# Kernel optimization log

Hardware: AMD Instinct MI355X
Metric: run time of the kernel (lower is better)

## Reference

```python
import jax, jax.numpy as jnp
import numpy as np

B, P, D, K = 16384, 20, 128, 5  # batch, nodes per sample, embed dim, knn k


def setup_inputs() -> dict:
    key = jax.random.key(0)
    ks = jax.random.split(key, 11)
    def rn(k, shape, scale=0.05):
        return jax.random.normal(k, shape, dtype=jnp.float32) * scale
    return {
        "x": jax.random.normal(ks[0], (B, P, D), dtype=jnp.float32),
        "W1": rn(ks[1], (300, D)), "b1": rn(ks[2], (300,)),
        "W2": rn(ks[3], (100, 300)), "b2": rn(ks[4], (100,)),
        "W3": rn(ks[5], (50, 100)), "b3": rn(ks[6], (50,)),
        "W4": rn(ks[7], (100, P * 50)), "b4": rn(ks[8], (100,)),
        "W5": rn(ks[9], (3, 100)), "b5": rn(ks[10], (3,)),
    }


def _gcn_agg_matrix(x, k):
    """Build the 20x20 GCN aggregation matrix equivalent to PyG GCNConv over the
    concatenated per-sample kNN edge lists (node ids shared 0..P-1 across batch)."""
    b, p, d = x.shape
    sq = jnp.sum(x * x, axis=-1)                                  # (B,P)
    d2 = sq[:, :, None] + sq[:, None, :] - 2.0 * jnp.einsum('bpd,bqd->bpq', x, x)
    d2 = jax.lax.stop_gradient(d2)  # indices only; squared dist preserves ordering
    _, idx = jax.lax.top_k(-d2, k + 1)                            # smallest k+1, sorted
    nbr = idx[..., 1:]                                            # (B,P,k) drop self
    src = jnp.broadcast_to(jnp.arange(p)[None, :, None], nbr.shape)
    flat = (nbr * p + src).reshape(-1)                            # C[v,u] multiplicity
    C = jnp.zeros((p * p,), jnp.float32).at[flat].add(1.0).reshape(p, p)
    deg = C.sum(axis=1) + 1.0                                     # in-degree + self-loop
    dinv = 1.0 / jnp.sqrt(deg)
    return dinv[:, None] * C * dinv[None, :] + jnp.diag(dinv * dinv)


def reference(x, W1, b1, W2, b2, W3, b3, W4, b4, W5, b5):
    h = x
    for W, b in ((W1, b1), (W2, b2), (W3, b3)):
        M = _gcn_agg_matrix(h, K)                                 # (P,P)
        h = jax.nn.relu(jnp.einsum('vu,bud->bvd', M, h @ W.T) + b)
    h = h.reshape(h.shape[0], -1)                                 # (B, P*50)
    h = jax.nn.relu(h @ W4.T + b4)
    logits = h @ W5.T + b5
    return jax.nn.softmax(logits, axis=1)
```

## Files before the change

### kernel.cpp

```cpp
#include <hip/hip_runtime.h>
#include <math.h>

#define BB 16384
#define P 20
#define NT 512

typedef short v8s __attribute__((ext_vector_type(8)));
typedef _Float16 v8h __attribute__((ext_vector_type(8)));
typedef float f32x4 __attribute__((ext_vector_type(4)));
typedef float f32x16 __attribute__((ext_vector_type(16)));

#define NELEM ((size_t)BB * P * 320)
__device__ unsigned int g_C[3][P * P];
__device__ __align__(16) unsigned short g_bufA[NELEM + 4096];
__device__ __align__(16) unsigned short g_bufB[NELEM + 4096];
__device__ __align__(16) unsigned short g_W1b[320 * 128];
__device__ __align__(16) unsigned short g_W2b[128 * 320];
__device__ __align__(16) unsigned short g_W3b[64 * 128];
__device__ __align__(16) unsigned short g_W4b[112 * 1024];
__device__ __align__(16) float g_b1p[320];
__device__ __align__(16) float g_b2p[128];
__device__ __align__(16) float g_b3p[64];
__device__ __align__(16) float g_b4p[112];

__device__ inline float bf2f(unsigned short u) {
    union { unsigned int i; float f; } c; c.i = ((unsigned int)u) << 16; return c.f;
}
__device__ inline unsigned short f2bf(float f) {
    union { float f; unsigned int i; } c; c.f = f;
    unsigned int u = c.i + 0x7fffu + ((c.i >> 16) & 1u);
    return (unsigned short)(u >> 16);
}

__global__ void zero_C_kernel() { g_C[blockIdx.x][threadIdx.x] = 0u; }

__global__ void prep_kernel(const float* __restrict__ W1, const float* __restrict__ b1,
                            const float* __restrict__ W2, const float* __restrict__ b2,
                            const float* __restrict__ W3, const float* __restrict__ b3,
                            const float* __restrict__ W4, const float* __restrict__ b4) {
    const int stride = gridDim.x * blockDim.x;
    const int id = blockIdx.x * blockDim.x + threadIdx.x;
    for (int i = id; i < 320 * 128; i += stride) { int n = i >> 7, k = i & 127;
        g_W1b[i] = (n < 300) ? f2bf(W1[n * 128 + k]) : 0; }
    for (int i = id; i < 128 * 320; i += stride) { int n = i / 320, k = i - n * 320;
        g_W2b[i] = (n < 100 && k < 300) ? f2bf(W2[n * 300 + k]) : 0; }
    for (int i = id; i < 64 * 128; i += stride) { int n = i >> 7, k = i & 127;
        g_W3b[i] = (n < 50 && k < 100) ? f2bf(W3[n * 100 + k]) : 0; }
    for (int i = id; i < 112 * 1024; i += stride) { int n = i >> 10, k = i & 1023;
        g_W4b[i] = (n < 100 && k < 1000) ? f2bf(W4[n * 1000 + k]) : 0; }
    for (int i = id; i < 320; i += stride) g_b1p[i] = (i < 300) ? b1[i] : 0.f;
    for (int i = id; i < 128; i += stride) g_b2p[i] = (i < 100) ? b2[i] : 0.f;
    for (int i = id; i < 64;  i += stride) g_b3p[i] = (i < 50)  ? b3[i] : 0.f;
    for (int i = id; i < 112; i += stride) g_b4p[i] = (i < 100) ? b4[i] : 0.f;
}

__global__ __launch_bounds__(NT)
void knn1_mfma_kernel(const float* __restrict__ x) {
    __shared__ float Gs[8][P * 21];
    __shared__ unsigned int hist[P * P];
    const int t = threadIdx.x, w = t >> 6, lane = t & 63;
    const int m31 = lane & 31, half = lane >> 5;
    const int mrow = (m31 < P) ? m31 : (P - 1);
    for (int i = t; i < P * P; i += NT) hist[i] = 0;
    for (int pass = 0; pass < 2; ++pass) {
        const size_t s = (size_t)blockIdx.x * 16 + pass * 8 + w;
        const float* rp = x + s * (size_t)(P * 128) + (size_t)mrow * 128 + half * 8;
        f32x16 acc;
#pragma unroll
        for (int i = 0; i < 16; ++i) acc[i] = 0.f;
#pragma unroll
        for (int ks = 0; ks < 8; ++ks) {
            float4 f0 = *(const float4*)(rp + ks * 16);
            float4 f1 = *(const float4*)(rp + ks * 16 + 4);
            float fv[8] = {f0.x, f0.y, f0.z, f0.w, f1.x, f1.y, f1.z, f1.w};
            v8h hi, lo;
#pragma unroll
            for (int j = 0; j < 8; ++j) {
                _Float16 hv = (_Float16)fv[j];
                hi[j] = hv;
                lo[j] = (_Float16)(fv[j] - (float)hv);
            }
            acc = __builtin_amdgcn_mfma_f32_32x32x16_f16(hi, hi, acc, 0, 0, 0);
            acc = __builtin_amdgcn_mfma_f32_32x32x16_f16(hi, lo, acc, 0, 0, 0);
            acc = __builtin_amdgcn_mfma_f32_32x32x16_f16(lo, hi, acc, 0, 0, 0);
            acc = __builtin_amdgcn_mfma_f32_32x32x16_f16(lo, lo, acc, 0, 0, 0);
        }
        float* G = &Gs[w][0];
        if (m31 < P) {
#pragma unroll
            for (int r = 0; r < 16; ++r) {
                int row = (r & 3) + 8 * (r >> 2) + 4 * half;
                if (row < P) G[row * 21 + m31] = acc[r];
            }
        }
        __syncthreads();
        if (lane < P) {
            const int p = lane;
            float d2[P];
            const float gpp = G[p * 21 + p];
#pragma unroll
            for (int u = 0; u < P; ++u)
                d2[u] = (u == p) ? 0.f : gpp + G[u * 21 + u] - 2.f * G[p * 21 + u];
            float pv = -3.0e38f; int pi = -1;
            for (int it = 0; it < 6; ++it) {
                float best = 3.0e38f; int bq = 0;
#pragma unroll
                for (int u = 0; u < P; ++u) {
                    float vu = d2[u];
                    bool cand = (vu > pv) || (vu == pv && u > pi);
                    if (cand && vu < best) { best = vu; bq = u; }
                }
                if (it > 0) atomicAdd(&hist[bq * P + p], 1u);
                pv = best; pi = bq;
            }
        }
        __syncthreads();
    }
    if (t < P * P && hist[t]) atomicAdd(&g_C[0][t], hist[t]);
}

template<int D, int CIDX>
__global__ __launch_bounds__(NT)
void knn_mfma_kernel() {
    __shared__ float Gs[8][P * 21];
    __shared__ unsigned int hist[P * P];
    const int t = threadIdx.x, w = t >> 6, lane = t & 63;
    const int m31 = lane & 31, half = lane >> 5;
    for (int i = t; i < P * P; i += NT) hist[i] = 0;
    for (int pass = 0; pass < 2; ++pass) {
        const size_t s = (size_t)blockIdx.x * 16 + pass * 8 + w;
        const unsigned short* rp = g_bufB + s * (P * D) + (size_t)m31 * D + half * 8;
        f32x16 acc;
#pragma unroll
        for (int i = 0; i < 16; ++i) acc[i] = 0.f;
        for (int ks = 0; ks < D / 16; ++ks) {
            v8s z = *(const v8s*)(rp + ks * 16);
            acc = __builtin_amdgcn_mfma_f32_32x32x16_bf16(z, z, acc, 0, 0, 0);
        }
        float* G = &Gs[w][0];
        if (m31 < P) {
#pragma unroll
            for (int r = 0; r < 16; ++r) {
                int row = (r & 3) + 8 * (r >> 2) + 4 * half;
                if (row < P) G[row * 21 + m31] = acc[r];
            }
        }
        __syncthreads();
        if (lane < P) {
            const int p = lane;
            float d2[P];
            const float gpp = G[p * 21 + p];
#pragma unroll
            for (int u = 0; u < P; ++u)
                d2[u] = (u == p) ? 0.f : gpp + G[u * 21 + u] - 2.f * G[p * 21 + u];
            float pv = -3.0e38f; int pi = -1;
            for (int it = 0; it < 6; ++it) {
                float best = 3.0e38f; int bq = 0;
#pragma unroll
                for (int u = 0; u < P; ++u) {
                    float vu = d2[u];
                    bool cand = (vu > pv) || (vu == pv && u > pi);
                    if (cand && vu < best) { best = vu; bq = u; }
                }
                if (it > 0) atomicAdd(&hist[bq * P + p], 1u);
                pv = best; pi = bq;
            }
        }
        __syncthreads();
    }
    if (t < P * P && hist[t]) atomicAdd(&g_C[CIDX][t], hist[t]);
}

__device__ inline void compute_M_512(const unsigned int* __restrict__ Cg,
                                     float* Ms, float* dinv, int t) {
    for (int i = t; i < P * P; i += 512) Ms[i] = (float)Cg[i];
    __syncthreads();
    if (t < P) {
        float deg = 1.f;
        for (int u = 0; u < P; ++u) deg += Ms[t * P + u];
        dinv[t] = 1.f / sqrtf(deg);
    }
    __syncthreads();
    for (int i = t; i < P * P; i += 512) {
        int v = i / P, u = i - v * P;
        float m = dinv[v] * Ms[i] * dinv[u];
        if (v == u) m += dinv[v] * dinv[v];
        Ms[i] = m;
    }
    __syncthreads();
}

template<int D, int CIDX>
__global__ __launch_bounds__(512)
void agg_mfma_kernel(const float* __restrict__ xin) {
    constexpr int NCB = D / 32;
    __shared__ float Ms[P * P];
    __shared__ float dinv[P];
    const int t = threadIdx.x, w = t >> 6, lane = t & 63;
    const int n31 = lane & 31, half = lane >> 5;
    compute_M_512(g_C[CIDX], Ms, dinv, t);
    v8s mhi[2], mlo[2];
#pragma unroll
    for (int kc = 0; kc < 2; ++kc)
#pragma unroll
        for (int j = 0; j < 8; ++j) {
            const int u = kc * 16 + half * 8 + j;
            const int v = n31;
            const float m = (v < P && u < P) ? Ms[v * P + u] : 0.f;
            const unsigned short h16 = f2bf(m);
            mhi[kc][j] = (short)h16;
            mlo[kc][j] = (short)f2bf(m - bf2f(h16));
        }
    const size_t s = (size_t)blockIdx.x * 8 + w;
    unsigned short* zout = g_bufA + s * (size_t)(P * D);
    const float* xr = xin + s * (size_t)(P * D);
#pragma unroll
    for (int cb = 0; cb < NCB; ++cb) {
        v8s bh0, bl0, bh1, bl1;
#pragma unroll
        for (int j = 0; j < 8; ++j) {
            const int u0 = half * 8 + j;
            int u1 = 16 + half * 8 + j; if (u1 > P - 1) u1 = P - 1;
            const float x0 = xr[(size_t)u0 * D + cb * 32 + n31];
            const float x1 = xr[(size_t)u1 * D + cb * 32 + n31];
            const unsigned short h0 = f2bf(x0), h1 = f2bf(x1);
            bh0[j] = (short)h0; bl0[j] = (short)f2bf(x0 - bf2f(h0));
            bh1[j] = (short)h1; bl1[j] = (short)f2bf(x1 - bf2f(h1));
        }
        f32x16 acc;
#pragma unroll
        for (int i = 0; i < 16; ++i) acc[i] = 0.f;
        acc = __builtin_amdgcn_mfma_f32_32x32x16_bf16(mhi[0], bh0, acc, 0, 0, 0);
        acc = __builtin_amdgcn_mfma_f32_32x32x16_bf16(mhi[0], bl0, acc, 0, 0, 0);
        acc = __builtin_amdgcn_mfma_f32_32x32x16_bf16(mlo[0], bh0, acc, 0, 0, 0);
        acc = __builtin_amdgcn_mfma_f32_32x32x16_bf16(mlo[0], bl0, acc, 0, 0, 0);
        acc = __builtin_amdgcn_mfma_f32_32x32x16_bf16(mhi[1], bh1, acc, 0, 0, 0);
        acc = __builtin_amdgcn_mfma_f32_32x32x16_bf16(mhi[1], bl1, acc, 0, 0, 0);
        acc = __builtin_amdgcn_mfma_f32_32x32x16_bf16(mlo[1], bh1, acc, 0, 0, 0);
        acc = __builtin_amdgcn_mfma_f32_32x32x16_bf16(mlo[1], bl1, acc, 0, 0, 0);
#pragma unroll
        for (int r = 0; r < 16; ++r) {
            const int row = (r & 3) + 8 * (r >> 2) + 4 * half;
            if (row < P)
                zout[(size_t)row * D + cb * 32 + n31] = f2bf(acc[r]);
        }
    }
}

template<int D, int CIDX, bool FLATOUT>
__global__ __launch_bounds__(512)
void agg_out_kernel() {
    constexpr int NCB = D / 32;
    __shared__ float Ms[P * P];
    __shared__ float dinv[P];
    const int t = threadIdx.x, w = t >> 6, lane = t & 63;
    const int n31 = lane & 31, half = lane >> 5;
    const float* __restrict__ bp = (CIDX == 1) ? g_b2p : g_b3p;
    compute_M_512(g_C[CIDX], Ms, dinv, t);
    v8s mhi[2], mlo[2];
#pragma unroll
    for (int kc = 0; kc < 2; ++kc)
#pragma unroll
        for (int j = 0; j < 8; ++j) {
            const int u = kc * 16 + half * 8 + j;
            const int v = n31;
            const float m = (v < P && u < P) ? Ms[v * P + u] : 0.f;
            const unsigned short h16 = f2bf(m);
            mhi[kc][j] = (short)h16;
            mlo[kc][j] = (short)f2bf(m - bf2f(h16));
        }
    const size_t s = (size_t)blockIdx.x * 8 + w;
    const float* yr = (const float*)g_bufA + s * (size_t)(P * D);
#pragma unroll
    for (int cb = 0; cb < NCB; ++cb) {
        v8s bh0, bl0, bh1, bl1;
#pragma unroll
        for (int j = 0; j < 8; ++j) {
            const int u0 = half * 8 + j;
            int u1 = 16 + half * 8 + j; if (u1 > P - 1) u1 = P - 1;
            const float x0 = yr[(size_t)u0 * D + cb * 32 + n31];
            const float x1 = yr[(size_t)u1 * D + cb * 32 + n31];
            const unsigned short h0 = f2bf(x0), h1 = f2bf(x1);
            bh0[j] = (short)h0; bl0[j] = (short)f2bf(x0 - bf2f(h0));
            bh1[j] = (short)h1; bl1[j] = (short)f2bf(x1 - bf2f(h1));
        }
        f32x16 acc;
#pragma unroll
        for (int i = 0; i < 16; ++i) acc[i] = 0.f;
        acc = __builtin_amdgcn_mfma_f32_32x32x16_bf16(mhi[0], bh0, acc, 0, 0, 0);
        acc = __builtin_amdgcn_mfma_f32_32x32x16_bf16(mhi[0], bl0, acc, 0, 0, 0);
        acc = __builtin_amdgcn_mfma_f32_32x32x16_bf16(mlo[0], bh0, acc, 0, 0, 0);
        acc = __builtin_amdgcn_mfma_f32_32x32x16_bf16(mlo[0], bl0, acc, 0, 0, 0);
        acc = __builtin_amdgcn_mfma_f32_32x32x16_bf16(mhi[1], bh1, acc, 0, 0, 0);
        acc = __builtin_amdgcn_mfma_f32_32x32x16_bf16(mhi[1], bl1, acc, 0, 0, 0);
        acc = __builtin_amdgcn_mfma_f32_32x32x16_bf16(mlo[1], bh1, acc, 0, 0, 0);
        acc = __builtin_amdgcn_mfma_f32_32x32x16_bf16(mlo[1], bl1, acc, 0, 0, 0);
        const float bv = bp[cb * 32 + n31];
#pragma unroll
        for (int r = 0; r < 16; ++r) {
            const int row = (r & 3) + 8 * (r >> 2) + 4 * half;
            if (row < P) {
                const float val = fmaxf(acc[r] + bv, 0.f);
                if (FLATOUT) {
                    const int d = cb * 32 + n31;
                    if (d < 50)
                        g_bufB[s * 1024 + (size_t)row * 50 + d] = f2bf(val);
                } else {
                    g_bufB[(s * (size_t)P + row) * D + cb * 32 + n31] = f2bf(val);
                }
            }
        }
    }
}

__global__ __launch_bounds__(256)
void gemm2_kernel() {
    constexpr int KL = 72;
    __shared__ __align__(16) unsigned short As[128 * KL];
    __shared__ __align__(16) unsigned short Wsh[128 * KL];
    const int t = threadIdx.x, w = t >> 6, lane = t & 63;
    const int m15 = lane & 15, q = lane >> 4;
    const long row0 = (long)blockIdx.x * 128;
    f32x4 acc[2][8];
#pragma unroll
    for (int zr = 0; zr < 2; ++zr)
#pragma unroll
        for (int nf = 0; nf < 8; ++nf) acc[zr][nf] = 0.f;
    for (int kc = 0; kc < 5; ++kc) {
        __syncthreads();
        for (int i = t; i < 1024; i += 256) {
            const int r = i >> 3, c8 = i & 7;
            *(v8s*)&As[r * KL + c8 * 8] =
                *(const v8s*)(g_bufB + (size_t)(row0 + r) * 320 + kc * 64 + c8 * 8);
            *(v8s*)&Wsh[r * KL + c8 * 8] =
                *(const v8s*)(g_W2b + (size_t)r * 320 + kc * 64 + c8 * 8);
        }
        __syncthreads();
#pragma unroll
        for (int ks = 0; ks < 2; ++ks) {
            v8s af[2];
#pragma unroll
            for (int zr = 0; zr < 2; ++zr)
                af[zr] = *(const v8s*)&As[(w * 32 + zr * 16 + m15) * KL + ks * 32 + q * 8];
#pragma unroll
            for (int nf = 0; nf < 8; ++nf) {
                v8s wf = *(const v8s*)&Wsh[(nf * 16 + m15) * KL + ks * 32 + q * 8];
#pragma unroll
                for (int zr = 0; zr < 2; ++zr)
                    acc[zr][nf] = __builtin_amdgcn_mfma_f32_16x16x32_bf16(
                        wf, af[zr], acc[zr][nf], 0, 0, 0);
            }
        }
    }
    float* yf = (float*)g_bufA;
#pragma unroll
    for (int zr = 0; zr < 2; ++zr) {
        const long m = row0 + w * 32 + zr * 16 + m15;
#pragma unroll
        for (int nf = 0; nf < 8; ++nf)
            *(f32x4*)(yf + (size_t)m * 128 + nf * 16 + q * 4) = acc[zr][nf];
    }
}

template<int Kp, int Np, int ZR, bool FLAT, int WSEL, bool ATOB, int NSPLIT,
         int KSC, int NTHR, long MROWS, bool RAWF32>
__global__ __launch_bounds__(NTHR)
void gemm_kernel() {
    constexpr int BN = Np / NSPLIT;
    constexpr int NF = BN / 16;
    constexpr int KS = Kp / 32;
    constexpr int CPT = KS / KSC;
    constexpr int KL = Kp + 8;
    constexpr int NW = NTHR / 64;
    constexpr int TM = NW * ZR * 16;
    constexpr long NTILE = MROWS / TM;
    static_assert(KS % KSC == 0, "KSC must divide KS");
    __shared__ __align__(16) unsigned short Ws[BN * KL];
    __shared__ __align__(16) float bs[BN];
    const unsigned short* __restrict__ Wb =
        (WSEL == 1) ? g_W1b : (WSEL == 2) ? g_W2b : (WSEL == 3) ? g_W3b : g_W4b;
    const float* __restrict__ bp =
        (WSEL == 1) ? g_b1p : (WSEL == 2) ? g_b2p : (WSEL == 3) ? g_b3p : g_b4p;
    const unsigned short* __restrict__ A = ATOB ? g_bufA : g_bufB;
    unsigned short* __restrict__ Hout = ATOB ? g_bufB : g_bufA;
    const int t = threadIdx.x, w = t >> 6, lane = t & 63;
    const int m15 = lane & 15, q = lane >> 4;
    const int n0 = blockIdx.y * BN;
    for (int i = t; i < BN * (Kp / 8); i += NTHR) {
        int r = i / (Kp / 8), c = i - r * (Kp / 8);
        *(v8s*)(&Ws[r * KL + c * 8]) = *(const v8s*)(Wb + (size_t)(n0 + r) * Kp + c * 8);
    }
    for (int i = t; i < BN; i += NTHR) bs[i] = bp[n0 + i];
    __syncthreads();

    v8s aC[ZR][KSC], aN[ZR][KSC];
    long tile = (long)blockIdx.x;
    if (tile < NTILE) {
        const unsigned short* ab =
            A + (size_t)(tile * TM + w * (ZR * 16) + m15) * Kp + q * 8;
#pragma unroll
        for (int zr = 0; zr < ZR; ++zr)
#pragma unroll
            for (int ks = 0; ks < KSC; ++ks)
                aC[zr][ks] = *(const v8s*)(ab + (size_t)zr * 16 * Kp + ks * 32);
    }
    for (; tile < NTILE; tile += gridDim.x) {
        f32x4 acc[ZR][NF];
#pragma unroll
        for (int zr = 0; zr < ZR; ++zr)
#pragma unroll
            for (int nf = 0; nf < NF; ++nf) acc[zr][nf] = 0.f;
        for (int c = 0; c < CPT; ++c) {
            const long ntile = (c + 1 < CPT) ? tile : tile + (long)gridDim.x;
            const int nk0 = (c + 1 < CPT) ? (c + 1) * KSC : 0;
            const bool hasNext = (ntile < NTILE);
            if (hasNext) {
                const unsigned short* ab =
                    A + (size_t)(ntile * TM + w * (ZR * 16) + m15) * Kp + nk0 * 32 + q * 8;
#pragma unroll
                for (int zr = 0; zr < ZR; ++zr)
#pragma unroll
                    for (int ks = 0; ks < KSC; ++ks)
                        aN[zr][ks] = *(const v8s*)(ab + (size_t)zr * 16 * Kp + ks * 32);
            }
#pragma unroll
            for (int nf = 0; nf < NF; ++nf) {
                v8s wr[KSC];
#pragma unroll
                for (int ks = 0; ks < KSC; ++ks)
                    wr[ks] = *(const v8s*)(&Ws[(nf * 16 + m15) * KL + (c * KSC + ks) * 32 + q * 8]);
#pragma unroll
                for (int ks = 0; ks < KSC; ++ks)
#pragma unroll
                    for (int zr = 0; zr < ZR; ++zr)
                        acc[zr][nf] = __builtin_amdgcn_mfma_f32_16x16x32_bf16(
                            wr[ks], aC[zr][ks], acc[zr][nf], 0, 0, 0);
            }
            if (hasNext) {
#pragma unroll
                for (int zr = 0; zr < ZR; ++zr)
#pragma unroll
                    for (int ks = 0; ks < KSC; ++ks) aC[zr][ks] = aN[zr][ks];
            }
        }
#pragma unroll
        for (int zr = 0; zr < ZR; ++zr) {
            const long m = tile * TM + w * (ZR * 16) + zr * 16 + m15;
#pragma unroll
            for (int nf = 0; nf < NF; ++nf) {
                f32x4 cc = acc[zr][nf];
                if (RAWF32) {
                    float* fH = (float*)Hout;
                    *(f32x4*)(fH + (size_t)m * Np + n0 + nf * 16 + q * 4) = cc;
                } else {
                    f32x4 b4 = *(const f32x4*)(&bs[nf * 16 + q * 4]);
                    float v0 = fmaxf(cc[0] + b4[0], 0.f), v1 = fmaxf(cc[1] + b4[1], 0.f);
                    float v2 = fmaxf(cc[2] + b4[2], 0.f), v3 = fmaxf(cc[3] + b4[3], 0.f);
                    if (!FLAT) {
                        ushort4 o; o.x = f2bf(v0); o.y = f2bf(v1); o.z = f2bf(v2); o.w = f2bf(v3);
                        *(ushort4*)(Hout + (size_t)m * Np + n0 + nf * 16 + q * 4) = o;
                    } else {
                        const int n0f = nf * 16 + q * 4;
                        if (n0f <= 48) {
                            const long s = m / 20; const int u = (int)(m - s * 20);
                            unsigned short* base = Hout + (size_t)s * 1024 + u * 50 + n0f;
                            unsigned int lo = (unsigned int)f2bf(v0) | ((unsigned int)f2bf(v1) << 16);
                            *(unsigned int*)(base) = lo;
                            if (n0f < 48) {
                                unsigned int hi = (unsigned int)f2bf(v2) | ((unsigned int)f2bf(v3) << 16);
                                *(unsigned int*)(base + 2) = hi;
                            }
                        }
                    }
                }
            }
        }
    }
}

__global__ __launch_bounds__(256)
void head_kernel(const float* __restrict__ W5, const float* __restrict__ b5,
                 float* __restrict__ out) {
    __shared__ float w5s[300];
    __shared__ float b5s[3];
    const int t = threadIdx.x;
    for (int i = t; i < 300; i += 256) w5s[i] = W5[i];
    if (t < 3) b5s[t] = b5[t];
    __syncthreads();
    const int s = blockIdx.x * 256 + t;
    const unsigned short* h = g_bufA + (size_t)s * 112;
    float a0 = b5s[0], a1 = b5s[1], a2 = b5s[2];
    for (int k = 0; k < 100; ++k) {
        float hv = bf2f(h[k]);
        a0 += hv * w5s[k]; a1 += hv * w5s[100 + k]; a2 += hv * w5s[200 + k];
    }
    float m = fmaxf(a0, fmaxf(a1, a2));
    float e0 = expf(a0 - m), e1 = expf(a1 - m), e2 = expf(a2 - m);
    float inv = 1.f / (e0 + e1 + e2);
    out[(size_t)s * 3 + 0] = e0 * inv;
    out[(size_t)s * 3 + 1] = e1 * inv;
    out[(size_t)s * 3 + 2] = e2 * inv;
}

extern "C" void kernel_launch(void* const* d_in, const int* in_sizes, int n_in,
                              void* d_out, int out_size, void* d_ws, size_t ws_size,
                              hipStream_t stream) {
    const float* x  = (const float*)d_in[0];
    const float* W1 = (const float*)d_in[1];
    const float* b1 = (const float*)d_in[2];
    const float* W2 = (const float*)d_in[3];
    const float* b2 = (const float*)d_in[4];
    const float* W3 = (const float*)d_in[5];
    const float* b3 = (const float*)d_in[6];
    const float* W4 = (const float*)d_in[7];
    const float* b4 = (const float*)d_in[8];
    const float* W5 = (const float*)d_in[9];
    const float* b5 = (const float*)d_in[10];
    float* out = (float*)d_out;

    zero_C_kernel<<<3, P * P, 0, stream>>>();
    prep_kernel<<<256, 256, 0, stream>>>(W1, b1, W2, b2, W3, b3, W4, b4);

    knn1_mfma_kernel<<<BB / 16, NT, 0, stream>>>(x);
    agg_mfma_kernel<128, 0><<<BB / 8, 512, 0, stream>>>(x);
    gemm_kernel<128, 320, 1, false, 1, true, 2, 4, 512, 327680L, false>
        <<<dim3(512, 2), 512, 0, stream>>>();

    knn_mfma_kernel<320, 1><<<BB / 16, NT, 0, stream>>>();
    gemm2_kernel<<<2560, 256, 0, stream>>>();
    agg_out_kernel<128, 1, false><<<BB / 8, 512, 0, stream>>>();

    knn_mfma_kernel<128, 2><<<BB / 16, NT, 0, stream>>>();
    gemm_kernel<128, 64, 2, false, 3, false, 1, 4, 256, 327680L, true>
        <<<dim3(512, 1), 256, 0, stream>>>();
    agg_out_kernel<64, 2, true><<<BB / 8, 512, 0, stream>>>();

    gemm_kernel<1024, 112, 1, false, 4, false, 7, 8, 256, 16384L, false>
        <<<dim3(256, 7), 256, 0, stream>>>();
    head_kernel<<<BB / 256, 256, 0, stream>>>(W5, b5, out);
}
```

Before: 861.8 us.

## Fuse layer-1 aggregation with W1 GEMM, keeping aggregated tile in LDS

Replaces the separate layer-1 aggregation kernel and the following W1 GEMM with one kernel. Each block aggregates four samples into shared memory, then multiplies them by a 160-column slice of W1 held in LDS, applying bias and ReLU before writing bf16 output. This removes the global write and re-read of the intermediate aggregated tensor and one launch. In exchange, aggregation is computed twice, once per column-half block (grid y=2), and the x reads double. Each block also reloads its W1 slice into LDS, and occupancy is lower because of the larger shared-memory use.

```diff
diff --git a/kernel.cpp b/kernel.cpp
--- a/kernel.cpp
+++ b/kernel.cpp
@@ -190,15 +190,17 @@
     __syncthreads();
 }
 
-template<int D, int CIDX>
 __global__ __launch_bounds__(512)
-void agg_mfma_kernel(const float* __restrict__ xin) {
-    constexpr int NCB = D / 32;
+void l1_fused_kernel(const float* __restrict__ x) {
     __shared__ float Ms[P * P];
     __shared__ float dinv[P];
+    __shared__ __align__(16) unsigned short Wsh[160 * 136];
+    __shared__ __align__(16) float bs[160];
+    __shared__ __align__(16) unsigned short zs[4][P][136];
     const int t = threadIdx.x, w = t >> 6, lane = t & 63;
     const int n31 = lane & 31, half = lane >> 5;
-    compute_M_512(g_C[CIDX], Ms, dinv, t);
+    const int n0 = blockIdx.y * 160;
+    compute_M_512(g_C[0], Ms, dinv, t);
     v8s mhi[2], mlo[2];
 #pragma unroll
     for (int kc = 0; kc < 2; ++kc)
@@ -211,21 +213,28 @@
             mhi[kc][j] = (short)h16;
             mlo[kc][j] = (short)f2bf(m - bf2f(h16));
         }
-    const size_t s = (size_t)blockIdx.x * 8 + w;
-    unsigned short* zout = g_bufA + s * (size_t)(P * D);
-    const float* xr = xin + s * (size_t)(P * D);
-#pragma unroll
-    for (int cb = 0; cb < NCB; ++cb) {
+    for (int i = t; i < 160 * 16; i += 512) {
+        const int r = i >> 4, c = i & 15;
+        *(v8s*)&Wsh[r * 136 + c * 8] =
+            *(const v8s*)(g_W1b + (size_t)(n0 + r) * 128 + c * 8);
+    }
+    for (int i = t; i < 160; i += 512) bs[i] = g_b1p[n0 + i];
+    const int smp = w >> 1, ch = w & 1;
+    const size_t s = (size_t)blockIdx.x * 4 + smp;
+    const float* xr = x + s * (size_t)(P * 128);
+#pragma unroll
+    for (int cbi = 0; cbi < 2; ++cbi) {
+        const int cb = ch * 2 + cbi;
         v8s bh0, bl0, bh1, bl1;
 #pragma unroll
         for (int j = 0; j < 8; ++j) {
             const int u0 = half * 8 + j;
             int u1 = 16 + half * 8 + j; if (u1 > P - 1) u1 = P - 1;
-            const float x0 = xr[(size_t)u0 * D + cb * 32 + n31];
-            const float x1 = xr[(size_t)u1 * D + cb * 32 + n31];
-            const unsigned short h0 = f2bf(x0), h1 = f2bf(x1);
+            const float x0 = xr[(size_t)u0 * 128 + cb * 32 + n31];
+            const float x1 = xr[(size_t)u1 * 128 + cb * 32 + n31];
+            const unsigned short h0 = f2bf(x0), h1v = f2bf(x1);
             bh0[j] = (short)h0; bl0[j] = (short)f2bf(x0 - bf2f(h0));
-            bh1[j] = (short)h1; bl1[j] = (short)f2bf(x1 - bf2f(h1));
+            bh1[j] = (short)h1v; bl1[j] = (short)f2bf(x1 - bf2f(h1v));
         }
         f32x16 acc;
 #pragma unroll
@@ -242,7 +251,44 @@
         for (int r = 0; r < 16; ++r) {
             const int row = (r & 3) + 8 * (r >> 2) + 4 * half;
             if (row < P)
-                zout[(size_t)row * D + cb * 32 + n31] = f2bf(acc[r]);
+                zs[smp][row][cb * 32 + n31] = f2bf(acc[r]);
+        }
+    }
+    __syncthreads();
+    const int nh = w & 1;
+    const int m15 = lane & 15, q = lane >> 4;
+    const int zrow0 = m15;
+    const int zrow1 = (16 + m15 < P) ? (16 + m15) : (P - 1);
+    f32x4 acc2[2][5];
+#pragma unroll
+    for (int zr = 0; zr < 2; ++zr)
+#pragma unroll
+        for (int nf = 0; nf < 5; ++nf) acc2[zr][nf] = 0.f;
+#pragma unroll
+    for (int ks = 0; ks < 4; ++ks) {
+        v8s z0 = *(const v8s*)&zs[smp][zrow0][ks * 32 + q * 8];
+        v8s z1f = *(const v8s*)&zs[smp][zrow1][ks * 32 + q * 8];
+#pragma unroll
+        for (int nf = 0; nf < 5; ++nf) {
+            v8s wf = *(const v8s*)&Wsh[(nh * 80 + nf * 16 + m15) * 136 + ks * 32 + q * 8];
+            acc2[0][nf] = __builtin_amdgcn_mfma_f32_16x16x32_bf16(wf, z0, acc2[0][nf], 0, 0, 0);
+            acc2[1][nf] = __builtin_amdgcn_mfma_f32_16x16x32_bf16(wf, z1f, acc2[1][nf], 0, 0, 0);
+        }
+    }
+#pragma unroll
+    for (int zr = 0; zr < 2; ++zr) {
+        const int vrow = zr * 16 + m15;
+        if (vrow < P) {
+#pragma unroll
+            for (int nf = 0; nf < 5; ++nf) {
+                f32x4 b4 = *(const f32x4*)&bs[nh * 80 + nf * 16 + q * 4];
+                f32x4 c = acc2[zr][nf];
+                float v0 = fmaxf(c[0] + b4[0], 0.f), v1 = fmaxf(c[1] + b4[1], 0.f);
+                float v2 = fmaxf(c[2] + b4[2], 0.f), v3 = fmaxf(c[3] + b4[3], 0.f);
+                ushort4 o; o.x = f2bf(v0); o.y = f2bf(v1); o.z = f2bf(v2); o.w = f2bf(v3);
+                *(ushort4*)(g_bufB + ((size_t)s * P + vrow) * 320 +
+                            n0 + nh * 80 + nf * 16 + q * 4) = o;
+            }
         }
     }
 }
@@ -522,9 +568,7 @@
     prep_kernel<<<256, 256, 0, stream>>>(W1, b1, W2, b2, W3, b3, W4, b4);
 
     knn1_mfma_kernel<<<BB / 16, NT, 0, stream>>>(x);
-    agg_mfma_kernel<128, 0><<<BB / 8, 512, 0, stream>>>(x);
-    gemm_kernel<128, 320, 1, false, 1, true, 2, 4, 512, 327680L, false>
-        <<<dim3(512, 2), 512, 0, stream>>>();
+    l1_fused_kernel<<<dim3(BB / 4, 2), 512, 0, stream>>>(x);
 
     knn_mfma_kernel<320, 1><<<BB / 16, NT, 0, stream>>>();
     gemm2_kernel<<<2560, 256, 0, stream>>>();
```

After: 880.4 us. 1.02x slower.

## Fuse layer-2/3 dense GEMM with GCN aggregation via LDS staging

Applied to the files above, without the earlier changes.

Replaces the separate GEMM (writing fp32 intermediates to global) and aggregation kernels for layers 2 and 3 with one kernel per layer. It computes a 160-row (8-sample) GEMM tile in LDS with 10 waves, then applies the 20x20 aggregation matrix from LDS and writes bf16 output. This removes the global round trip of the fp32 intermediate and one launch per layer. In exchange the GEMM tile is smaller, weights are reloaded per block, occupancy drops because LDS use is large (~67KB), and the buffers now ping-pong between A and B.

```diff
diff --git a/kernel.cpp b/kernel.cpp
--- a/kernel.cpp
+++ b/kernel.cpp
@@ -119,17 +119,18 @@
     if (t < P * P && hist[t]) atomicAdd(&g_C[0][t], hist[t]);
 }
 
-template<int D, int CIDX>
+template<int D, int CIDX, bool IN_A>
 __global__ __launch_bounds__(NT)
 void knn_mfma_kernel() {
     __shared__ float Gs[8][P * 21];
     __shared__ unsigned int hist[P * P];
     const int t = threadIdx.x, w = t >> 6, lane = t & 63;
     const int m31 = lane & 31, half = lane >> 5;
+    const unsigned short* __restrict__ hb = IN_A ? g_bufA : g_bufB;
     for (int i = t; i < P * P; i += NT) hist[i] = 0;
     for (int pass = 0; pass < 2; ++pass) {
         const size_t s = (size_t)blockIdx.x * 16 + pass * 8 + w;
-        const unsigned short* rp = g_bufB + s * (P * D) + (size_t)m31 * D + half * 8;
+        const unsigned short* rp = hb + s * (P * D) + (size_t)m31 * D + half * 8;
         f32x16 acc;
 #pragma unroll
         for (int i = 0; i < 16; ++i) acc[i] = 0.f;
@@ -247,16 +248,38 @@
     }
 }
 
-template<int D, int CIDX, bool FLATOUT>
-__global__ __launch_bounds__(512)
-void agg_out_kernel() {
-    constexpr int NCB = D / 32;
+template<int Kp, int Np, int CIDX, bool FLATOUT, bool IN_A>
+__global__ __launch_bounds__(640)
+void l23_fused_kernel() {
+    constexpr int NHALF = Np / 64;
+    constexpr int KC = Kp / 64;
     __shared__ float Ms[P * P];
     __shared__ float dinv[P];
+    __shared__ __align__(16) unsigned short As[160 * 72];
+    __shared__ __align__(16) unsigned short Wsh[64 * 72];
+    __shared__ __align__(16) float yls[160][68];
     const int t = threadIdx.x, w = t >> 6, lane = t & 63;
     const int n31 = lane & 31, half = lane >> 5;
+    const int m15 = lane & 15, q = lane >> 4;
+    const unsigned short* __restrict__ hin = IN_A ? g_bufA : g_bufB;
+    unsigned short* __restrict__ hout = IN_A ? g_bufB : g_bufA;
+    const unsigned short* __restrict__ Wb = (CIDX == 1) ? g_W2b : g_W3b;
     const float* __restrict__ bp = (CIDX == 1) ? g_b2p : g_b3p;
-    compute_M_512(g_C[CIDX], Ms, dinv, t);
+    for (int i = t; i < P * P; i += 640) Ms[i] = (float)g_C[CIDX][i];
+    __syncthreads();
+    if (t < P) {
+        float deg = 1.f;
+        for (int u = 0; u < P; ++u) deg += Ms[t * P + u];
+        dinv[t] = 1.f / sqrtf(deg);
+    }
+    __syncthreads();
+    for (int i = t; i < P * P; i += 640) {
+        int v = i / P, u = i - v * P;
+        float m = dinv[v] * Ms[i] * dinv[u];
+        if (v == u) m += dinv[v] * dinv[v];
+        Ms[i] = m;
+    }
+    __syncthreads();
     v8s mhi[2], mlo[2];
 #pragma unroll
     for (int kc = 0; kc < 2; ++kc)
@@ -269,96 +292,80 @@
             mhi[kc][j] = (short)h16;
             mlo[kc][j] = (short)f2bf(m - bf2f(h16));
         }
-    const size_t s = (size_t)blockIdx.x * 8 + w;
-    const float* yr = (const float*)g_bufA + s * (size_t)(P * D);
-#pragma unroll
-    for (int cb = 0; cb < NCB; ++cb) {
-        v8s bh0, bl0, bh1, bl1;
-#pragma unroll
-        for (int j = 0; j < 8; ++j) {
-            const int u0 = half * 8 + j;
-            int u1 = 16 + half * 8 + j; if (u1 > P - 1) u1 = P - 1;
-            const float x0 = yr[(size_t)u0 * D + cb * 32 + n31];
-            const float x1 = yr[(size_t)u1 * D + cb * 32 + n31];
-            const unsigned short h0 = f2bf(x0), h1 = f2bf(x1);
-            bh0[j] = (short)h0; bl0[j] = (short)f2bf(x0 - bf2f(h0));
-            bh1[j] = (short)h1; bl1[j] = (short)f2bf(x1 - bf2f(h1));
-        }
-        f32x16 acc;
-#pragma unroll
-        for (int i = 0; i < 16; ++i) acc[i] = 0.f;
-        acc = __builtin_amdgcn_mfma_f32_32x32x16_bf16(mhi[0], bh0, acc, 0, 0, 0);
-        acc = __builtin_amdgcn_mfma_f32_32x32x16_bf16(mhi[0], bl0, acc, 0, 0, 0);
-        acc = __builtin_amdgcn_mfma_f32_32x32x16_bf16(mlo[0], bh0, acc, 0, 0, 0);
-        acc = __builtin_amdgcn_mfma_f32_32x32x16_bf16(mlo[0], bl0, acc, 0, 0, 0);
-        acc = __builtin_amdgcn_mfma_f32_32x32x16_bf16(mhi[1], bh1, acc, 0, 0, 0);
-        acc = __builtin_amdgcn_mfma_f32_32x32x16_bf16(mhi[1], bl1, acc, 0, 0, 0);
-        acc = __builtin_amdgcn_mfma_f32_32x32x16_bf16(mlo[1], bh1, acc, 0, 0, 0);
-        acc = __builtin_amdgcn_mfma_f32_32x32x16_bf16(mlo[1], bl1, acc, 0, 0, 0);
-        const float bv = bp[cb * 32 + n31];
-#pragma unroll
-        for (int r = 0; r < 16; ++r) {
-            const int row = (r & 3) + 8 * (r >> 2) + 4 * half;
-            if (row < P) {
-                const float val = fmaxf(acc[r] + bv, 0.f);
-                if (FLATOUT) {
-                    const int d = cb * 32 + n31;
-                    if (d < 50)
-                        g_bufB[s * 1024 + (size_t)row * 50 + d] = f2bf(val);
-                } else {
-                    g_bufB[(s * (size_t)P + row) * D + cb * 32 + n31] = f2bf(val);
+    const long row0 = (long)blockIdx.x * 160;
+    for (int nh = 0; nh < NHALF; ++nh) {
+        f32x4 acc[4];
+#pragma unroll
+        for (int nf = 0; nf < 4; ++nf) acc[nf] = 0.f;
+        for (int kc = 0; kc < KC; ++kc) {
+            __syncthreads();
+            for (int i = t; i < 1280; i += 640) {
+                const int r = i >> 3, c8 = i & 7;
+                *(v8s*)&As[r * 72 + c8 * 8] =
+                    *(const v8s*)(hin + (size_t)(row0 + r) * Kp + kc * 64 + c8 * 8);
+            }
+            for (int i = t; i < 512; i += 640) {
+                const int r = i >> 3, c8 = i & 7;
+                *(v8s*)&Wsh[r * 72 + c8 * 8] =
+                    *(const v8s*)(Wb + (size_t)(nh * 64 + r) * Kp + kc * 64 + c8 * 8);
+            }
+            __syncthreads();
+#pragma unroll
+            for (int ks = 0; ks < 2; ++ks) {
+                v8s af = *(const v8s*)&As[(w * 16 + m15) * 72 + ks * 32 + q * 8];
+#pragma unroll
+                for (int nf = 0; nf < 4; ++nf) {
+                    v8s wf = *(const v8s*)&Wsh[(nf * 16 + m15) * 72 + ks * 32 + q * 8];
+                    acc[nf] = __builtin_amdgcn_mfma_f32_16x16x32_bf16(
+                        wf, af, acc[nf], 0, 0, 0);
                 }
             }
         }
-    }
-}
-
-__global__ __launch_bounds__(256)
-void gemm2_kernel() {
-    constexpr int KL = 72;
-    __shared__ __align__(16) unsigned short As[128 * KL];
-    __shared__ __align__(16) unsigned short Wsh[128 * KL];
-    const int t = threadIdx.x, w = t >> 6, lane = t & 63;
-    const int m15 = lane & 15, q = lane >> 4;
-    const long row0 = (long)blockIdx.x * 128;
-    f32x4 acc[2][8];
-#pragma unroll
-    for (int zr = 0; zr < 2; ++zr)
-#pragma unroll
-        for (int nf = 0; nf < 8; ++nf) acc[zr][nf] = 0.f;
-    for (int kc = 0; kc < 5; ++kc) {
+#pragma unroll
+        for (int nf = 0; nf < 4; ++nf)
+            *(f32x4*)&yls[w * 16 + m15][nf * 16 + q * 4] = acc[nf];
         __syncthreads();
-        for (int i = t; i < 1024; i += 256) {
-            const int r = i >> 3, c8 = i & 7;
-            *(v8s*)&As[r * KL + c8 * 8] =
-                *(const v8s*)(g_bufB + (size_t)(row0 + r) * 320 + kc * 64 + c8 * 8);
-            *(v8s*)&Wsh[r * KL + c8 * 8] =
-                *(const v8s*)(g_W2b + (size_t)r * 320 + kc * 64 + c8 * 8);
-        }
-        __syncthreads();
-#pragma unroll
-        for (int ks = 0; ks < 2; ++ks) {
-            v8s af[2];
-#pragma unroll
-            for (int zr = 0; zr < 2; ++zr)
-                af[zr] = *(const v8s*)&As[(w * 32 + zr * 16 + m15) * KL + ks * 32 + q * 8];
-#pragma unroll
-            for (int nf = 0; nf < 8; ++nf) {
-                v8s wf = *(const v8s*)&Wsh[(nf * 16 + m15) * KL + ks * 32 + q * 8];
-#pragma unroll
-                for (int zr = 0; zr < 2; ++zr)
-                    acc[zr][nf] = __builtin_amdgcn_mfma_f32_16x16x32_bf16(
-                        wf, af[zr], acc[zr][nf], 0, 0, 0);
-            }
-        }
-    }
-    float* yf = (float*)g_bufA;
-#pragma unroll
-    for (int zr = 0; zr < 2; ++zr) {
-        const long m = row0 + w * 32 + zr * 16 + m15;
-#pragma unroll
-        for (int nf = 0; nf < 8; ++nf)
-            *(f32x4*)(yf + (size_t)m * 128 + nf * 16 + q * 4) = acc[zr][nf];
+        for (int task = w; task < 16; task += 10) {
+            const int smp = task >> 1, cb = task & 1;
+            const size_t s = (size_t)blockIdx.x * 8 + smp;
+            v8s bh0, bl0, bh1, bl1;
+#pragma unroll
+            for (int j = 0; j < 8; ++j) {
+                const int u0 = half * 8 + j;
+                int u1 = 16 + half * 8 + j; if (u1 > P - 1) u1 = P - 1;
+                const float x0 = yls[smp * 20 + u0][cb * 32 + n31];
+                const float x1 = yls[smp * 20 + u1][cb * 32 + n31];
+                const unsigned short h0 = f2bf(x0), h1 = f2bf(x1);
+                bh0[j] = (short)h0; bl0[j] = (short)f2bf(x0 - bf2f(h0));
+                bh1[j] = (short)h1; bl1[j] = (short)f2bf(x1 - bf2f(h1));
+            }
+            f32x16 acc2;
+#pragma unroll
+            for (int i = 0; i < 16; ++i) acc2[i] = 0.f;
+            acc2 = __builtin_amdgcn_mfma_f32_32x32x16_bf16(mhi[0], bh0, acc2, 0, 0, 0);
+            acc2 = __builtin_amdgcn_mfma_f32_32x32x16_bf16(mhi[0], bl0, acc2, 0, 0, 0);
+            acc2 = __builtin_amdgcn_mfma_f32_32x32x16_bf16(mlo[0], bh0, acc2, 0, 0, 0);
+            acc2 = __builtin_amdgcn_mfma_f32_32x32x16_bf16(mlo[0], bl0, acc2, 0, 0, 0);
+            acc2 = __builtin_amdgcn_mfma_f32_32x32x16_bf16(mhi[1], bh1, acc2, 0, 0, 0);
+            acc2 = __builtin_amdgcn_mfma_f32_32x32x16_bf16(mhi[1], bl1, acc2, 0, 0, 0);
+            acc2 = __builtin_amdgcn_mfma_f32_32x32x16_bf16(mlo[1], bh1, acc2, 0, 0, 0);
+            acc2 = __builtin_amdgcn_mfma_f32_32x32x16_bf16(mlo[1], bl1, acc2, 0, 0, 0);
+            const int dl = cb * 32 + n31;
+            const float bv = bp[nh * 64 + dl];
+#pragma unroll
+            for (int r = 0; r < 16; ++r) {
+                const int row = (r & 3) + 8 * (r >> 2) + 4 * half;
+                if (row < P) {
+                    const float val = fmaxf(acc2[r] + bv, 0.f);
+                    if (FLATOUT) {
+                        if (dl < 50)
+                            hout[s * 1024 + (size_t)row * 50 + dl] = f2bf(val);
+                    } else {
+                        hout[(s * (size_t)P + row) * Np + nh * 64 + dl] = f2bf(val);
+                    }
+                }
+            }
+        }
     }
 }
 
@@ -526,14 +533,13 @@
     gemm_kernel<128, 320, 1, false, 1, true, 2, 4, 512, 327680L, false>
         <<<dim3(512, 2), 512, 0, stream>>>();
 
-    knn_mfma_kernel<320, 1><<<BB / 16, NT, 0, stream>>>();
-    gemm2_kernel<<<2560, 256, 0, stream>>>();
-    agg_out_kernel<128, 1, false><<<BB / 8, 512, 0, stream>>>();
-
-    knn_mfma_kernel<128, 2><<<BB / 16, NT, 0, stream>>>();
-    gemm_kernel<128, 64, 2, false, 3, false, 1, 4, 256, 327680L, true>
-        <<<dim3(512, 1), 256, 0, stream>>>();
-    agg_out_kernel<64, 2, true><<<BB / 8, 512, 0, stream>>>();
+    knn_mfma_kernel<320, 1, false><<<BB / 16, NT, 0, stream>>>();
+    l23_fused_kernel<320, 128, 1, false, false>
+        <<<BB / 8, 640, 0, stream>>>();
+
+    knn_mfma_kernel<128, 2, true><<<BB / 16, NT, 0, stream>>>();
+    l23_fused_kernel<128, 64, 2, true, true>
+        <<<BB / 8, 640, 0, stream>>>();
 
     gemm_kernel<1024, 112, 1, false, 4, false, 7, 8, 256, 16384L, false>
         <<<dim3(256, 7), 256, 0, stream>>>();
```

Result: slower. 912.5 us (+5.9%).
